# Optimization experiments

Measured on AMD Instinct MI355X. Metric: run time of the kernel, lower is better.

## Reference

```python
import jax, jax.numpy as jnp
import numpy as np

B, T, A, H, E = 512, 64, 32, 512, 32


def sinusoidal_pos_encoding(t, dim):
    # t: (B, T) float positions -> (B, T, dim)
    half = dim // 2
    freqs = jnp.exp(-jnp.log(10000.0) * jnp.arange(half, dtype=jnp.float32) / half)
    ang = t[..., None] * freqs  # (B, T, half)
    return jnp.concatenate([jnp.sin(ang), jnp.cos(ang)], axis=-1)


def cat_linear(x, W, b, cat_ids):
    # x: (B, T, Din); W: (E, Din, Dout); b: (E, Dout); cat_ids: (B,)
    Wg = W[cat_ids]            # (B, Din, Dout) gathered per-sample weights
    bg = b[cat_ids][:, None]   # (B, 1, Dout)
    return jnp.einsum('btd,bdh->bth', x, Wg) + bg


def swish(x):
    return x * jax.nn.sigmoid(x)


def setup_inputs() -> dict:
    key = jax.random.key(0)
    ks = jax.random.split(key, 10)
    s = lambda fan_in: 1.0 / np.sqrt(fan_in)
    return {
        'actions': jax.random.normal(ks[0], (B, T, A), dtype=jnp.float32),
        'timesteps': jax.random.uniform(ks[1], (B,), dtype=jnp.float32),
        'cat_ids': jax.random.randint(ks[2], (B,), 0, E),
        'W1': jax.random.normal(ks[3], (E, A, H), dtype=jnp.float32) * s(A),
        'b1': jnp.zeros((E, H), dtype=jnp.float32),
        'W2': jax.random.normal(ks[4], (E, 2 * H, H), dtype=jnp.float32) * s(2 * H),
        'b2': jnp.zeros((E, H), dtype=jnp.float32),
        'W3': jax.random.normal(ks[5], (E, H, H), dtype=jnp.float32) * s(H),
        'b3': jnp.zeros((E, H), dtype=jnp.float32),
    }


def reference(actions, timesteps, cat_ids, W1, b1, W2, b2, W3, b3):
    b, t, _ = actions.shape
    timesteps_bt = jnp.broadcast_to(timesteps[:, None], (b, t))
    a_emb = cat_linear(actions, W1, b1, cat_ids)              # (B, T, H)
    tau_emb = sinusoidal_pos_encoding(timesteps_bt, H).astype(a_emb.dtype)
    x = jnp.concatenate([a_emb, tau_emb], axis=-1)            # (B, T, 2H)
    x = swish(cat_linear(x, W2, b2, cat_ids))                 # (B, T, H)
    x = cat_linear(x, W3, b3, cat_ids)                        # (B, T, H)
    return x
```

## Files before the change

### kernel.cpp

```cpp
#include <hip/hip_runtime.h>
#include <hip/hip_bf16.h>

#define B_ 512
#define T_ 64
#define A_ 32
#define H_ 512
#define E_ 32
#define MAX_TASKS 272

typedef unsigned short u16;
typedef unsigned int u32;
typedef __attribute__((ext_vector_type(8))) short short8;
typedef __attribute__((ext_vector_type(4))) float floatx4;

static __device__ __forceinline__ u16 f2bf(float f) {
    u32 u = __builtin_bit_cast(u32, f);
    u += 0x7fffu + ((u >> 16) & 1u);
    return (u16)(u >> 16);
}

__global__ void group_kernel(const int* __restrict__ cat_ids,
                             int* __restrict__ sample_list,
                             int4* __restrict__ tasks) {
    __shared__ int cnt[E_], off[E_], cur[E_], toff[E_];
    __shared__ int total;
    int tid = threadIdx.x;
    if (tid < E_) { cnt[tid] = 0; cur[tid] = 0; }
    __syncthreads();
    int e = cat_ids[tid];
    atomicAdd(&cnt[e], 1);
    __syncthreads();
    if (tid == 0) {
        int run = 0, trun = 0;
        for (int i = 0; i < E_; i++) {
            off[i] = run;  run += cnt[i];
            toff[i] = trun; trun += (cnt[i] + 1) >> 1;
        }
        total = trun;
    }
    __syncthreads();
    if (tid < E_) {
        int c = cnt[tid], o = off[tid], to = toff[tid];
        for (int j = 0; j < c; j += 2)
            tasks[to++] = make_int4(tid, o + j, (c - j >= 2) ? 2 : 1, 0);
    }
    for (int i = total + tid; i < MAX_TASKS; i += 512)
        tasks[i] = make_int4(0, 0, 0, 0);
    int p = atomicAdd(&cur[e], 1);
    sample_list[off[e] + p] = tid;
}

__global__ __launch_bounds__(256) void embed_kernel(
        const float* __restrict__ actions, const float* __restrict__ timesteps,
        const int* __restrict__ cat_ids, const float* __restrict__ W1,
        const float* __restrict__ b1, u16* __restrict__ a_emb,
        u16* __restrict__ tau_emb) {
    int b = blockIdx.x;
    int tid = threadIdx.x;
    int e = cat_ids[b];
    float tval = timesteps[b];

    {
        float freq = expf(-9.210340371976184f * (float)tid * (1.0f / 256.0f));
        float ang = tval * freq;
        tau_emb[b * H_ + tid]       = f2bf(sinf(ang));
        tau_emb[b * H_ + 256 + tid] = f2bf(cosf(ang));
    }

    __shared__ float act[T_ * A_];
    const float* asrc = actions + (size_t)b * T_ * A_;
    for (int i = tid; i < T_ * A_; i += 256) act[i] = asrc[i];
    __syncthreads();

    const float* w1 = W1 + (size_t)e * A_ * H_;
    int n0 = tid, n1 = tid + 256;
    float wA[A_], wB[A_];
#pragma unroll
    for (int k = 0; k < A_; k++) {
        wA[k] = w1[k * H_ + n0];
        wB[k] = w1[k * H_ + n1];
    }
    float bA = b1[e * H_ + n0], bB = b1[e * H_ + n1];
    u16* orow = a_emb + (size_t)b * T_ * H_;
    for (int tt = 0; tt < T_; tt++) {
        float accA = bA, accB = bB;
#pragma unroll
        for (int k = 0; k < A_; k++) {
            float a = act[tt * A_ + k];
            accA = fmaf(a, wA[k], accA);
            accB = fmaf(a, wB[k], accB);
        }
        orow[tt * H_ + n0] = f2bf(accA);
        orow[tt * H_ + n1] = f2bf(accB);
    }
}

__global__ __launch_bounds__(256) void convert_transpose(
        const float* __restrict__ W, u16* __restrict__ Wt, int K) {
    int n = blockIdx.y * 256 + threadIdx.x;
    int k0 = blockIdx.x * 32;
    int e = blockIdx.z;
    const float* src = W + ((size_t)e * K + k0) * H_ + n;
    short8 out[4];
#pragma unroll
    for (int j = 0; j < 32; j++)
        out[j >> 3][j & 7] = (short)f2bf(src[(size_t)j * H_]);
    u16* dst = Wt + ((size_t)e * H_ + n) * K + k0;
#pragma unroll
    for (int c = 0; c < 4; c++) *(short8*)(dst + c * 8) = out[c];
}

#define LDSTR 72

template <int DIN, bool HAS_TAU, bool DO_SWISH, bool OUT_BF16>
__global__ __launch_bounds__(256, 3) void moe_gemm(
        const u16* __restrict__ xsrc, const u16* __restrict__ tau,
        const u16* __restrict__ Wt, const float* __restrict__ bias,
        const int* __restrict__ sample_list, const int4* __restrict__ tasks,
        void* __restrict__ outp) {
    int4 task = tasks[blockIdx.y];
    int ns = task.z;
    if (ns == 0) return;
    int e = task.x;
    int s0 = sample_list[task.y];
    int s1 = (ns > 1) ? sample_list[task.y + 1] : s0;
    int n0 = blockIdx.x * 128;

    int tid = threadIdx.x;
    int lane = tid & 63, wv = tid >> 6;
    int wr = wv >> 1, wc = wv & 1;
    int quad = lane >> 4, c15 = lane & 15;

    __shared__ __align__(16) u16 xs[128 * LDSTR];
    __shared__ __align__(16) u16 wt[128 * LDSTR];

    floatx4 acc[4][4];
    floatx4 zero4 = {0.f, 0.f, 0.f, 0.f};
#pragma unroll
    for (int i = 0; i < 4; i++)
#pragma unroll
        for (int j = 0; j < 4; j++) acc[i][j] = zero4;

    const u16* wbase = Wt + (size_t)(e * H_ + n0) * DIN;
    int sr = tid >> 2;
    int sk = (tid & 3) * 16;

    for (int k0 = 0; k0 < DIN; k0 += 64) {
        bool use_tau = HAS_TAU && (k0 >= 512);
#pragma unroll
        for (int h = 0; h < 2; h++) {
            int row = sr + h * 64;
            int s = (row < 64) ? s0 : s1;
            int t = row & 63;
            const u16* src = use_tau
                ? (tau + (size_t)s * H_ + (k0 - 512) + sk)
                : (xsrc + ((size_t)s * T_ + t) * H_ + k0 + sk);
            *(short8*)&xs[row * LDSTR + sk]     = *(const short8*)src;
            *(short8*)&xs[row * LDSTR + sk + 8] = *(const short8*)(src + 8);
        }
#pragma unroll
        for (int h = 0; h < 2; h++) {
            int nn = sr + h * 64;
            const u16* src = wbase + (size_t)nn * DIN + k0 + sk;
            *(short8*)&wt[nn * LDSTR + sk]     = *(const short8*)src;
            *(short8*)&wt[nn * LDSTR + sk + 8] = *(const short8*)(src + 8);
        }
        __syncthreads();

#pragma unroll
        for (int kk = 0; kk < 2; kk++) {
            short8 af[4], bfr[4];
#pragma unroll
            for (int i = 0; i < 4; i++) {
                af[i]  = *(const short8*)&xs[(wr * 64 + i * 16 + c15) * LDSTR + kk * 32 + quad * 8];
                bfr[i] = *(const short8*)&wt[(wc * 64 + i * 16 + c15) * LDSTR + kk * 32 + quad * 8];
            }
#pragma unroll
            for (int mt = 0; mt < 4; mt++)
#pragma unroll
                for (int nt = 0; nt < 4; nt++)
                    acc[mt][nt] = __builtin_amdgcn_mfma_f32_16x16x32_bf16(
                            af[mt], bfr[nt], acc[mt][nt], 0, 0, 0);
        }
        __syncthreads();
    }

    const float* bp = bias + (size_t)e * H_;
#pragma unroll
    for (int mt = 0; mt < 4; mt++) {
        int rbase = wr * 64 + mt * 16 + quad * 4;
        int side = rbase >> 6;
        if (side == 1 && ns == 1) continue;
        int s = side ? s1 : s0;
#pragma unroll
        for (int nt = 0; nt < 4; nt++) {
            int col = n0 + wc * 64 + nt * 16 + c15;
            float bv = bp[col];
#pragma unroll
            for (int r = 0; r < 4; r++) {
                int t = (rbase + r) & 63;
                float v = acc[mt][nt][r] + bv;
                if (DO_SWISH) v = v / (1.0f + expf(-v));
                size_t oidx = ((size_t)s * T_ + t) * H_ + col;
                if (OUT_BF16) ((u16*)outp)[oidx] = f2bf(v);
                else          ((float*)outp)[oidx] = v;
            }
        }
    }
}

extern "C" void kernel_launch(void* const* d_in, const int* in_sizes, int n_in,
                              void* d_out, int out_size, void* d_ws, size_t ws_size,
                              hipStream_t stream) {
    const float* actions   = (const float*)d_in[0];
    const float* timesteps = (const float*)d_in[1];
    const int*   cat_ids   = (const int*)d_in[2];
    const float* W1 = (const float*)d_in[3];
    const float* b1 = (const float*)d_in[4];
    const float* W2 = (const float*)d_in[5];
    const float* b2 = (const float*)d_in[6];
    const float* W3 = (const float*)d_in[7];
    const float* b3 = (const float*)d_in[8];

    char* ws = (char*)d_ws;
    u16* a_emb = (u16*)ws;
    u16* y     = (u16*)(ws + (size_t)32 * 1024 * 1024);
    u16* tau   = (u16*)(ws + (size_t)64 * 1024 * 1024);
    int* sample_list = (int*)(ws + (size_t)64 * 1024 * 1024 + 512 * 1024);
    int4* tasks = (int4*)(ws + (size_t)64 * 1024 * 1024 + 512 * 1024 + 4096);
    u16* Wt2 = (u16*)d_out;
    u16* Wt3 = a_emb;

    hipLaunchKernelGGL(group_kernel, dim3(1), dim3(512), 0, stream,
                       cat_ids, sample_list, tasks);
    hipLaunchKernelGGL(embed_kernel, dim3(512), dim3(256), 0, stream,
                       actions, timesteps, cat_ids, W1, b1, a_emb, tau);
    hipLaunchKernelGGL(convert_transpose, dim3(2 * H_ / 32, 2, E_), dim3(256),
                       0, stream, W2, Wt2, 2 * H_);
    hipLaunchKernelGGL((moe_gemm<2 * H_, true, true, true>), dim3(4, MAX_TASKS),
                       dim3(256), 0, stream,
                       a_emb, tau, Wt2, b2, sample_list, tasks, (void*)y);
    hipLaunchKernelGGL(convert_transpose, dim3(H_ / 32, 2, E_), dim3(256),
                       0, stream, W3, Wt3, H_);
    hipLaunchKernelGGL((moe_gemm<H_, false, false, false>), dim3(4, MAX_TASKS),
                       dim3(256), 0, stream,
                       y, (const u16*)nullptr, Wt3, b3, sample_list, tasks, d_out);
}
```

Baseline: 351.8 us.

## Group four samples per MoE GEMM block with direct global-to-LDS swizzled loads

Each task now covers up to four samples of the same expert instead of two, and the block grows to 512 threads with a 256-row tile. Each weight tile is therefore reused across twice as many rows and fewer blocks re-read the same expert weights. Staging moves to global_load_lds with an XOR-swizzled layout in place of the padded LDS stride, to avoid register round-trips and bank conflicts. In exchange, experts with few samples leave more idle rows per block, and the larger LDS and thread footprint may lower occupancy.

```diff
diff --git a/kernel.cpp b/kernel.cpp
--- a/kernel.cpp
+++ b/kernel.cpp
@@ -6,7 +6,7 @@
 #define A_ 32
 #define H_ 512
 #define E_ 32
-#define MAX_TASKS 272
+#define MAX_TASKS 160
 
 typedef unsigned short u16;
 typedef unsigned int u32;
@@ -17,6 +17,12 @@
     u32 u = __builtin_bit_cast(u32, f);
     u += 0x7fffu + ((u >> 16) & 1u);
     return (u16)(u >> 16);
+}
+
+static __device__ __forceinline__ void gl2lds16(const u16* g, u16* l) {
+    __builtin_amdgcn_global_load_lds(
+        (const __attribute__((address_space(1))) void*)g,
+        (__attribute__((address_space(3))) void*)l, 16, 0, 0);
 }
 
 __global__ void group_kernel(const int* __restrict__ cat_ids,
@@ -34,15 +40,17 @@
         int run = 0, trun = 0;
         for (int i = 0; i < E_; i++) {
             off[i] = run;  run += cnt[i];
-            toff[i] = trun; trun += (cnt[i] + 1) >> 1;
+            toff[i] = trun; trun += (cnt[i] + 3) >> 2;
         }
         total = trun;
     }
     __syncthreads();
     if (tid < E_) {
         int c = cnt[tid], o = off[tid], to = toff[tid];
-        for (int j = 0; j < c; j += 2)
-            tasks[to++] = make_int4(tid, o + j, (c - j >= 2) ? 2 : 1, 0);
+        for (int j = 0; j < c; j += 4) {
+            int ns = c - j; if (ns > 4) ns = 4;
+            tasks[to++] = make_int4(tid, o + j, ns, 0);
+        }
     }
     for (int i = total + tid; i < MAX_TASKS; i += 512)
         tasks[i] = make_int4(0, 0, 0, 0);
@@ -110,10 +118,8 @@
     for (int c = 0; c < 4; c++) *(short8*)(dst + c * 8) = out[c];
 }
 
-#define LDSTR 72
-
 template <int DIN, bool HAS_TAU, bool DO_SWISH, bool OUT_BF16>
-__global__ __launch_bounds__(256, 3) void moe_gemm(
+__global__ __launch_bounds__(512, 4) void moe_gemm(
         const u16* __restrict__ xsrc, const u16* __restrict__ tau,
         const u16* __restrict__ Wt, const float* __restrict__ bias,
         const int* __restrict__ sample_list, const int4* __restrict__ tasks,
@@ -122,17 +128,20 @@
     int ns = task.z;
     if (ns == 0) return;
     int e = task.x;
-    int s0 = sample_list[task.y];
-    int s1 = (ns > 1) ? sample_list[task.y + 1] : s0;
+    int sl[4];
+#pragma unroll
+    for (int j = 0; j < 4; j++)
+        sl[j] = sample_list[task.y + ((j < ns) ? j : (ns - 1))];
     int n0 = blockIdx.x * 128;
 
     int tid = threadIdx.x;
     int lane = tid & 63, wv = tid >> 6;
     int wr = wv >> 1, wc = wv & 1;
     int quad = lane >> 4, c15 = lane & 15;
-
-    __shared__ __align__(16) u16 xs[128 * LDSTR];
-    __shared__ __align__(16) u16 wt[128 * LDSTR];
+    int r8 = lane >> 3, cg = lane & 7;
+
+    __shared__ __align__(16) u16 xs[256 * 64];
+    __shared__ __align__(16) u16 wt[128 * 64];
 
     floatx4 acc[4][4];
     floatx4 zero4 = {0.f, 0.f, 0.f, 0.f};
@@ -142,38 +151,39 @@
         for (int j = 0; j < 4; j++) acc[i][j] = zero4;
 
     const u16* wbase = Wt + (size_t)(e * H_ + n0) * DIN;
-    int sr = tid >> 2;
-    int sk = (tid & 3) * 16;
+    int kc_sw = (cg ^ r8) * 8;
 
     for (int k0 = 0; k0 < DIN; k0 += 64) {
         bool use_tau = HAS_TAU && (k0 >= 512);
 #pragma unroll
-        for (int h = 0; h < 2; h++) {
-            int row = sr + h * 64;
-            int s = (row < 64) ? s0 : s1;
-            int t = row & 63;
-            const u16* src = use_tau
-                ? (tau + (size_t)s * H_ + (k0 - 512) + sk)
-                : (xsrc + ((size_t)s * T_ + t) * H_ + k0 + sk);
-            *(short8*)&xs[row * LDSTR + sk]     = *(const short8*)src;
-            *(short8*)&xs[row * LDSTR + sk + 8] = *(const short8*)(src + 8);
-        }
-#pragma unroll
-        for (int h = 0; h < 2; h++) {
-            int nn = sr + h * 64;
-            const u16* src = wbase + (size_t)nn * DIN + k0 + sk;
-            *(short8*)&wt[nn * LDSTR + sk]     = *(const short8*)src;
-            *(short8*)&wt[nn * LDSTR + sk + 8] = *(const short8*)(src + 8);
+        for (int j = 0; j < 4; j++) {
+            int rg = 8 * wv + 64 * j;
+            int t = 8 * wv + r8;
+            int s = sl[j];
+            const u16* g = use_tau
+                ? (tau + (size_t)s * H_ + (k0 - 512) + kc_sw)
+                : (xsrc + ((size_t)s * T_ + t) * H_ + k0 + kc_sw);
+            gl2lds16(g, &xs[rg * 64]);
+        }
+#pragma unroll
+        for (int i = 0; i < 2; i++) {
+            int ng = 8 * wv + 64 * i;
+            int nrow = ng + r8;
+            const u16* g = wbase + (size_t)nrow * DIN + k0 + kc_sw;
+            gl2lds16(g, &wt[ng * 64]);
         }
         __syncthreads();
 
 #pragma unroll
         for (int kk = 0; kk < 2; kk++) {
+            int c = kk * 4 + quad;
             short8 af[4], bfr[4];
 #pragma unroll
             for (int i = 0; i < 4; i++) {
-                af[i]  = *(const short8*)&xs[(wr * 64 + i * 16 + c15) * LDSTR + kk * 32 + quad * 8];
-                bfr[i] = *(const short8*)&wt[(wc * 64 + i * 16 + c15) * LDSTR + kk * 32 + quad * 8];
+                int row = wr * 64 + i * 16 + c15;
+                af[i] = *(const short8*)&xs[row * 64 + ((c ^ (row & 7)) * 8)];
+                int nr = wc * 64 + i * 16 + c15;
+                bfr[i] = *(const short8*)&wt[nr * 64 + ((c ^ (nr & 7)) * 8)];
             }
 #pragma unroll
             for (int mt = 0; mt < 4; mt++)
@@ -185,23 +195,21 @@
         __syncthreads();
     }
 
+    if (wr >= ns) return;
+    int s = sl[wr];
     const float* bp = bias + (size_t)e * H_;
 #pragma unroll
     for (int mt = 0; mt < 4; mt++) {
-        int rbase = wr * 64 + mt * 16 + quad * 4;
-        int side = rbase >> 6;
-        if (side == 1 && ns == 1) continue;
-        int s = side ? s1 : s0;
+        int tb = mt * 16 + quad * 4;
 #pragma unroll
         for (int nt = 0; nt < 4; nt++) {
             int col = n0 + wc * 64 + nt * 16 + c15;
             float bv = bp[col];
 #pragma unroll
             for (int r = 0; r < 4; r++) {
-                int t = (rbase + r) & 63;
                 float v = acc[mt][nt][r] + bv;
                 if (DO_SWISH) v = v / (1.0f + expf(-v));
-                size_t oidx = ((size_t)s * T_ + t) * H_ + col;
+                size_t oidx = ((size_t)s * T_ + tb + r) * H_ + col;
                 if (OUT_BF16) ((u16*)outp)[oidx] = f2bf(v);
                 else          ((float*)outp)[oidx] = v;
             }
@@ -238,11 +246,11 @@
     hipLaunchKernelGGL(convert_transpose, dim3(2 * H_ / 32, 2, E_), dim3(256),
                        0, stream, W2, Wt2, 2 * H_);
     hipLaunchKernelGGL((moe_gemm<2 * H_, true, true, true>), dim3(4, MAX_TASKS),
-                       dim3(256), 0, stream,
+                       dim3(512), 0, stream,
                        a_emb, tau, Wt2, b2, sample_list, tasks, (void*)y);
     hipLaunchKernelGGL(convert_transpose, dim3(H_ / 32, 2, E_), dim3(256),
                        0, stream, W3, Wt3, H_);
     hipLaunchKernelGGL((moe_gemm<H_, false, false, false>), dim3(4, MAX_TASKS),
-                       dim3(256), 0, stream,
+                       dim3(512), 0, stream,
                        y, (const u16*)nullptr, Wt3, b3, sample_list, tasks, d_out);
 }
```

New measurement: 323.0 us. 1.09x faster.
